# Kernel tuning notes

Measured on AMD Instinct MI355X. Metric: run time of the kernel, lower is better.

The kernel has to match this reference:

```python
import jax, jax.numpy as jnp
import numpy as np

B, N, DIM = 4, 2048, 1024
HEADS, DH = 16, 64
INNER = HEADS * DH
SCALE = 8.0
EPS = 1e-5


def setup_inputs() -> dict:
    key = jax.random.key(0)
    ks = jax.random.split(key, 8)
    x = jax.random.normal(ks[0], (B, N, DIM), dtype=jnp.float32)
    context_mask = jax.random.bernoulli(ks[1], 0.9, (B, N))
    gamma = jnp.ones((DIM,), dtype=jnp.float32)
    null_kv = jax.random.normal(ks[2], (2, HEADS, 1, DH), dtype=jnp.float32)
    Wq = jax.random.normal(ks[3], (DIM, INNER), dtype=jnp.float32) * 0.02
    Wkv = jax.random.normal(ks[4], (DIM, 2 * INNER), dtype=jnp.float32) * 0.02
    # q_scale init: scale / dim_head**-0.5 = 8 * sqrt(64) = 64
    q_scale = jnp.full((DH,), SCALE * (DH ** 0.5), dtype=jnp.float32)
    k_scale = jnp.ones((DH,), dtype=jnp.float32)
    Wout = jax.random.normal(ks[5], (INNER, DIM), dtype=jnp.float32) * 0.02
    return {"x": x, "context_mask": context_mask, "gamma": gamma,
            "null_kv": null_kv, "Wq": Wq, "Wkv": Wkv,
            "q_scale": q_scale, "k_scale": k_scale, "Wout": Wout}


def _l2norm(t):
    return t / jnp.sqrt(jnp.sum(t * t, axis=-1, keepdims=True) + 1e-12)


def reference(x, context_mask, gamma, null_kv, Wq, Wkv, q_scale, k_scale, Wout):
    b, n, _ = x.shape
    # LayerNorm (beta buffer is zeros)
    mu = jnp.mean(x, axis=-1, keepdims=True)
    var = jnp.mean((x - mu) ** 2, axis=-1, keepdims=True)
    xn = (x - mu) / jnp.sqrt(var + EPS) * gamma
    # projections
    q = (xn @ Wq).reshape(b, n, HEADS, DH)
    kv = xn @ Wkv
    k = kv[..., :INNER].reshape(b, n, HEADS, DH)
    v = kv[..., INNER:].reshape(b, n, HEADS, DH)
    # null kv token: [h,1,d] -> [b,1,h,d]
    nk = jnp.broadcast_to(null_kv[0].transpose(1, 0, 2)[None], (b, 1, HEADS, DH))
    nv = jnp.broadcast_to(null_kv[1].transpose(1, 0, 2)[None], (b, 1, HEADS, DH))
    k = jnp.concatenate([nk, k], axis=1)  # [b, n+1, h, d]
    v = jnp.concatenate([nv, v], axis=1)
    # cosine-sim attention with learned per-dim scales
    q = _l2norm(q) * q_scale
    k = _l2norm(k) * k_scale
    # bias from mask (padded True for null token)
    mask = jnp.pad(context_mask, ((0, 0), (1, 0)), constant_values=True)
    bias = jnp.where(mask, 0.0, -10000.0)[:, None, None, :]  # [b,1,1,n+1]
    # memory_efficient_attention applies 1/sqrt(dh) internally
    scores = jnp.einsum('bqhd,bkhd->bhqk', q, k) * (DH ** -0.5) + bias
    attn = jax.nn.softmax(scores, axis=-1)
    out = jnp.einsum('bhqk,bkhd->bqhd', attn, v).reshape(b, n, INNER)
    return out @ Wout
```

## Files before the change

kernel.cpp:

```cpp
#include <hip/hip_runtime.h>
#include <hip/hip_bf16.h>
#include <stdint.h>


using f32x4  = __attribute__((ext_vector_type(4))) float;
using bf16x8 = __attribute__((ext_vector_type(8))) __bf16;
using f16x8  = __attribute__((ext_vector_type(8))) _Float16;
using uintv4 = __attribute__((ext_vector_type(4))) unsigned int;

__device__ __forceinline__ float b2f(unsigned short u) {
    return __uint_as_float(((unsigned)u) << 16);
}
__device__ __forceinline__ unsigned short f2b(float f) {
    unsigned u = __float_as_uint(f);
    u += 0x7fffu + ((u >> 16) & 1u);
    return (unsigned short)(u >> 16);
}
__device__ __forceinline__ f32x4 mfma16(bf16x8 a, bf16x8 b, f32x4 c) {
    return __builtin_amdgcn_mfma_f32_16x16x32_bf16(a, b, c, 0, 0, 0);
}
__device__ __forceinline__ f32x4 mfma16h(f16x8 a, f16x8 b, f32x4 c) {
    return __builtin_amdgcn_mfma_f32_16x16x32_f16(a, b, c, 0, 0, 0);
}
__device__ __forceinline__ unsigned pk16(float a, float b) {
    return __builtin_bit_cast(unsigned, __builtin_amdgcn_cvt_pkrtz(a, b));
}
__device__ __forceinline__ void gl_lds16(const unsigned short* g, __bf16* l) {
    __builtin_amdgcn_global_load_lds(
        (const __attribute__((address_space(1))) unsigned int*)g,
        (__attribute__((address_space(3))) unsigned int*)l, 16, 0, 0);
}

__global__ __launch_bounds__(256) void transpose_f2b(
    const float* __restrict__ in, unsigned short* __restrict__ out,
    int R, int C)
{
    __shared__ unsigned short t[32][33];
    int tx = threadIdx.x, ty = threadIdx.y;
    int c = blockIdx.x * 32 + tx;
#pragma unroll
    for (int i = 0; i < 4; ++i) {
        int r = blockIdx.y * 32 + ty + i * 8;
        t[ty + i * 8][tx] = f2b(in[(size_t)r * C + c]);
    }
    __syncthreads();
    int r2 = blockIdx.y * 32 + tx;
#pragma unroll
    for (int i = 0; i < 4; ++i) {
        int c2 = blockIdx.x * 32 + ty + i * 8;
        out[(size_t)c2 * R + r2] = t[tx][ty + i * 8];
    }
}

__global__ __launch_bounds__(256) void ln_kernel(
    const float* __restrict__ x, const float* __restrict__ gamma,
    unsigned short* __restrict__ xn)
{
    int row = blockIdx.x, tid = threadIdx.x;
    int wave = tid >> 6, lane = tid & 63;
    float4 raw = *(const float4*)(x + ((size_t)row << 10) + (tid << 2));
    float v[4] = { raw.x, raw.y, raw.z, raw.w };
    float s  = v[0] + v[1] + v[2] + v[3];
    float s2 = v[0]*v[0] + v[1]*v[1] + v[2]*v[2] + v[3]*v[3];
#pragma unroll
    for (int off = 1; off < 64; off <<= 1) {
        s  += __shfl_xor(s, off);
        s2 += __shfl_xor(s2, off);
    }
    __shared__ float ps[4], ps2[4], sh[2];
    if (lane == 0) { ps[wave] = s; ps2[wave] = s2; }
    __syncthreads();
    if (tid == 0) {
        float S  = ps[0] + ps[1] + ps[2] + ps[3];
        float S2 = ps2[0] + ps2[1] + ps2[2] + ps2[3];
        float mu  = S * (1.f / 1024.f);
        float var = S2 * (1.f / 1024.f) - mu * mu;
        sh[0] = mu; sh[1] = rsqrtf(var + 1e-5f);
    }
    __syncthreads();
    float mu = sh[0], rstd = sh[1];
    float4 g4 = *(const float4*)(gamma + (tid << 2));
    float g[4] = { g4.x, g4.y, g4.z, g4.w };
    unsigned short o[4];
#pragma unroll
    for (int i = 0; i < 4; ++i) o[i] = f2b((v[i] - mu) * rstd * g[i]);
    uint2 out;
    out.x = (unsigned)o[0] | ((unsigned)o[1] << 16);
    out.y = (unsigned)o[2] | ((unsigned)o[3] << 16);
    *(uint2*)(xn + ((size_t)row << 10) + (tid << 2)) = out;
}

template<int MODE>
__global__ __launch_bounds__(256, 2) void gemm_bt(
    const unsigned short* __restrict__ A, const unsigned short* __restrict__ Bt,
    void* __restrict__ Cout, const float* __restrict__ scale,
    int M, int N, int K)
{
    __shared__ __bf16 As[128 * 32];
    __shared__ __bf16 Bs[128 * 32];
    int tid = threadIdx.x, lane = tid & 63, wave = tid >> 6;
    int quad = lane >> 4, l15 = lane & 15;
    int m0 = blockIdx.y * 128, n0 = blockIdx.x * 128;
    int wm = (wave & 1) * 64, wn = (wave >> 1) * 64;
    f32x4 acc[4][4] = {};

    const int srow = wave * 32 + (lane >> 2);
    const int scol = (lane & 3) << 3;
    const unsigned short* gA = A  + (size_t)(m0 + srow) * K + scol;
    const unsigned short* gB = Bt + (size_t)(n0 + srow) * K + scol;
    __bf16* lA0 = &As[(wave * 32) * 32];
    __bf16* lA1 = &As[(wave * 32 + 16) * 32];
    __bf16* lB0 = &Bs[(wave * 32) * 32];
    __bf16* lB1 = &Bs[(wave * 32 + 16) * 32];
    const size_t rstep = (size_t)16 * K;

    for (int k0 = 0; k0 < K; k0 += 32) {
        gl_lds16(gA,         lA0);
        gl_lds16(gA + rstep, lA1);
        gl_lds16(gB,         lB0);
        gl_lds16(gB + rstep, lB1);
        gA += 32; gB += 32;
        __syncthreads();
        bf16x8 af[4], bfv[4];
#pragma unroll
        for (int i = 0; i < 4; ++i)
            af[i] = *(const bf16x8*)&As[(wm + i * 16 + l15) * 32 + quad * 8];
#pragma unroll
        for (int j = 0; j < 4; ++j)
            bfv[j] = *(const bf16x8*)&Bs[(wn + j * 16 + l15) * 32 + quad * 8];
#pragma unroll
        for (int i = 0; i < 4; ++i)
#pragma unroll
            for (int j = 0; j < 4; ++j)
                acc[i][j] = mfma16(af[i], bfv[j], acc[i][j]);
        __syncthreads();
    }

    if (MODE == 2) {
#pragma unroll
        for (int i = 0; i < 4; ++i)
#pragma unroll
            for (int j = 0; j < 4; ++j) {
                int row = m0 + wm + i * 16 + quad * 4;
                int col = n0 + wn + j * 16 + l15;
                size_t base = (size_t)row * N + col;
#pragma unroll
                for (int r = 0; r < 4; ++r)
                    ((float*)Cout)[base + (size_t)r * N] = acc[i][j][r];
            }
        return;
    }

    const bool isv = (MODE == 1) && ((n0 + wn) >= 1024);
    float sc[4];
    if (!isv) {
#pragma unroll
        for (int j = 0; j < 4; ++j) {
            float s = scale[j * 16 + l15];
            sc[j] = (MODE == 0) ? s * (0.125f * 1.44269504088896f) : s;
        }
    }
#pragma unroll
    for (int i = 0; i < 4; ++i)
#pragma unroll
        for (int r = 0; r < 4; ++r) {
            float mul = 1.f;
            if (!isv) {
                float ss = 0.f;
#pragma unroll
                for (int j = 0; j < 4; ++j) ss += acc[i][j][r] * acc[i][j][r];
                ss += __shfl_xor(ss, 1); ss += __shfl_xor(ss, 2);
                ss += __shfl_xor(ss, 4); ss += __shfl_xor(ss, 8);
                mul = rsqrtf(ss + 1e-12f);
            }
            size_t rowbase = (size_t)(m0 + wm + i * 16 + quad * 4 + r) * N
                           + n0 + wn + l15;
#pragma unroll
            for (int j = 0; j < 4; ++j) {
                float v = acc[i][j][r];
                unsigned short w = isv
                    ? __builtin_bit_cast(unsigned short, (_Float16)v)
                    : f2b(v * mul * sc[j]);
                ((unsigned short*)Cout)[rowbase + j * 16] = w;
            }
        }
}

__global__ __launch_bounds__(256) void nullkv_kernel(
    const float* __restrict__ null_kv, const float* __restrict__ k_scale,
    unsigned short* __restrict__ knull, unsigned short* __restrict__ vnull)
{
    int wave = threadIdx.x >> 6, lane = threadIdx.x & 63;
    int h = blockIdx.x * 4 + wave;
    int idx = (h << 6) + lane;
    float kvl = null_kv[idx];
    float ss = kvl * kvl;
#pragma unroll
    for (int off = 1; off < 64; off <<= 1) ss += __shfl_xor(ss, off);
    knull[idx] = f2b(kvl * rsqrtf(ss + 1e-12f) * k_scale[lane]);
    vnull[idx] = __builtin_bit_cast(unsigned short, (_Float16)null_kv[1024 + idx]);
}

__global__ __launch_bounds__(256, 3) void attn_kernel(
    const unsigned short* __restrict__ qn,
    const unsigned short* __restrict__ kv,
    const unsigned short* __restrict__ knull,
    const unsigned short* __restrict__ vnull,
    const int* __restrict__ mask,
    unsigned short* __restrict__ ao)
{
    __shared__ __bf16 Kt[2][64 * 64];
    __shared__ unsigned int Vt32[64 * 34];
    __shared__ __align__(16) float biasLds[64];

    const int tid = threadIdx.x, lane = tid & 63, wave = tid >> 6;
    const int quad = lane >> 4, l15 = lane & 15;
    const int bh = blockIdx.x;
    const int b = bh >> 4, h = bh & 15;
    const int mbase = blockIdx.y * 128 + wave * 32;
    const size_t rowoff = (size_t)b * 2048;

    bf16x8 qf[2][2];
#pragma unroll
    for (int rg = 0; rg < 2; ++rg)
#pragma unroll
        for (int ks = 0; ks < 2; ++ks)
            qf[rg][ks] = *(const bf16x8*)
                &qn[((rowoff + mbase + rg * 16 + l15) << 10) + (h << 6) + ks * 32 + quad * 8];

    const int t8  = lane >> 3;
    const int ksc = ((lane & 7) ^ t8) << 3;

    uint2 va[2], vb[2]; float vmsk;

    auto kIssue = [&](int nt, int buf) {
#pragma unroll
        for (int p = 0; p < 2; ++p) {
            int r = wave * 16 + p * 8 + t8;
            int T = ((r >> 5) << 5) | (((r >> 2) & 3) << 3)
                  | (((r >> 4) & 1) << 2) | (r & 3);
            int j = (nt << 6) + T;
            int jr = j - 1; if (jr > 2047) jr = 2047;
            const unsigned short* src = (j == 0)
                ? knull + (h << 6) + ksc
                : kv + ((rowoff + (size_t)jr) << 11) + (h << 6) + ksc;
            gl_lds16(src, &Kt[buf][(wave * 16 + p * 8) * 64]);
        }
    };
    auto vPrefetch = [&](int nt) {
#pragma unroll
        for (int it = 0; it < 2; ++it) {
            int u = it * 256 + tid;
            int tp = u >> 4, d0 = (u & 15) << 2;
            int j0 = (nt << 6) + tp * 2;
            int jr0 = j0 - 1; if (jr0 > 2047) jr0 = 2047;
            int jr1 = j0;     if (jr1 > 2047) jr1 = 2047;
            const unsigned short* s0 = (j0 == 0)
                ? vnull + (h << 6) + d0
                : kv + ((rowoff + (size_t)jr0) << 11) + 1024 + (h << 6) + d0;
            const unsigned short* s1 =
                  kv + ((rowoff + (size_t)jr1) << 11) + 1024 + (h << 6) + d0;
            va[it] = *(const uint2*)s0;
            vb[it] = *(const uint2*)s1;
        }
        int j = (nt << 6) + tid;
        float bv = -512.f;
        if (j == 0 || (j <= 2048 && mask[b * 2048 + j - 1] != 0)) bv = 0.f;
        vmsk = bv;
    };
    auto vCommit = [&]() {
#pragma unroll
        for (int it = 0; it < 2; ++it) {
            int u = it * 256 + tid;
            int tp = u >> 4, d0 = (u & 15) << 2;
            unsigned ax = va[it].x, ay = va[it].y;
            unsigned bx = vb[it].x, by = vb[it].y;
            Vt32[(d0 + 0) * 34 + tp] = (ax & 0xffffu) | (bx << 16);
            Vt32[(d0 + 1) * 34 + tp] = (ax >> 16)     | (bx & 0xffff0000u);
            Vt32[(d0 + 2) * 34 + tp] = (ay & 0xffffu) | (by << 16);
            Vt32[(d0 + 3) * 34 + tp] = (ay >> 16)     | (by & 0xffff0000u);
        }
        if (tid < 64) biasLds[tid] = vmsk;
    };

    f32x4 O[2][4] = {};
    float rs[2] = {0.f, 0.f};

    kIssue(0, 0);
    vPrefetch(0);

    for (int nt = 0; nt < 33; ++nt) {
        const int buf = nt & 1;
        __syncthreads();
        vCommit();
        __syncthreads();
        if (nt < 32) {
            kIssue(nt + 1, buf ^ 1);
            vPrefetch(nt + 1);
        }

#pragma unroll
        for (int g = 0; g < 2; ++g) {
            float4 b0 = *(const float4*)&biasLds[(g << 5) + (quad << 3)];
            float4 b1 = *(const float4*)&biasLds[(g << 5) + (quad << 3) + 4];
            f32x4 s[2][2];
#pragma unroll
            for (int rg = 0; rg < 2; ++rg) {
                s[rg][0] = f32x4{ b0.x, b0.y, b0.z, b0.w };
                s[rg][1] = f32x4{ b1.x, b1.y, b1.z, b1.w };
            }
#pragma unroll
            for (int t = 0; t < 2; ++t) {
                const __bf16* kb = &Kt[buf][((g * 2 + t) * 16 + l15) * 64];
                bf16x8 k0 = *(const bf16x8*)&kb[(quad ^ (l15 & 7)) << 3];
                bf16x8 k1 = *(const bf16x8*)&kb[((4 + quad) ^ (l15 & 7)) << 3];
#pragma unroll
                for (int rg = 0; rg < 2; ++rg) {
                    s[rg][t] = mfma16(k0, qf[rg][0], s[rg][t]);
                    s[rg][t] = mfma16(k1, qf[rg][1], s[rg][t]);
                }
            }
            f16x8 vf8[4];
#pragma unroll
            for (int dt = 0; dt < 4; ++dt) {
                int cu = (dt * 16 + l15) * 34 + (g << 4) + (quad << 2);
                uint2 lo = *(const uint2*)&Vt32[cu];
                uint2 hi = *(const uint2*)&Vt32[cu + 2];
                uintv4 rv = { lo.x, lo.y, hi.x, hi.y };
                vf8[dt] = __builtin_bit_cast(f16x8, rv);
            }
#pragma unroll
            for (int rg = 0; rg < 2; ++rg) {
                float e0 = __builtin_amdgcn_exp2f(s[rg][0][0]);
                float e1 = __builtin_amdgcn_exp2f(s[rg][0][1]);
                float e2 = __builtin_amdgcn_exp2f(s[rg][0][2]);
                float e3 = __builtin_amdgcn_exp2f(s[rg][0][3]);
                float e4 = __builtin_amdgcn_exp2f(s[rg][1][0]);
                float e5 = __builtin_amdgcn_exp2f(s[rg][1][1]);
                float e6 = __builtin_amdgcn_exp2f(s[rg][1][2]);
                float e7 = __builtin_amdgcn_exp2f(s[rg][1][3]);
                rs[rg] += ((e0 + e1) + (e2 + e3)) + ((e4 + e5) + (e6 + e7));
                uintv4 pu = { pk16(e0, e1), pk16(e2, e3),
                              pk16(e4, e5), pk16(e6, e7) };
                f16x8 p = __builtin_bit_cast(f16x8, pu);
#pragma unroll
                for (int dt = 0; dt < 4; ++dt)
                    O[rg][dt] = mfma16h(p, vf8[dt], O[rg][dt]);
            }
        }
    }

#pragma unroll
    for (int rg = 0; rg < 2; ++rg) {
        rs[rg] += __shfl_xor(rs[rg], 16);
        rs[rg] += __shfl_xor(rs[rg], 32);
    }
#pragma unroll
    for (int rg = 0; rg < 2; ++rg) {
        float inv[4];
#pragma unroll
        for (int r = 0; r < 4; ++r)
            inv[r] = 1.f / __shfl(rs[rg], quad * 4 + r);
#pragma unroll
        for (int dt = 0; dt < 4; ++dt) {
            size_t base = ((rowoff + mbase + rg * 16 + quad * 4) << 10)
                        + (h << 6) + dt * 16 + l15;
#pragma unroll
            for (int r = 0; r < 4; ++r)
                ao[base + ((size_t)r << 10)] = f2b(O[rg][dt][r] * inv[r]);
        }
    }
}

extern "C" void kernel_launch(void* const* d_in, const int* in_sizes, int n_in,
                              void* d_out, int out_size, void* d_ws, size_t ws_size,
                              hipStream_t stream)
{
    const float* x       = (const float*)d_in[0];
    const int*   mask    = (const int*)d_in[1];
    const float* gamma   = (const float*)d_in[2];
    const float* null_kv = (const float*)d_in[3];
    const float* Wq      = (const float*)d_in[4];
    const float* Wkv     = (const float*)d_in[5];
    const float* q_scale = (const float*)d_in[6];
    const float* k_scale = (const float*)d_in[7];
    const float* Wout    = (const float*)d_in[8];

    char* ws = (char*)d_ws;
    unsigned short* xn    = (unsigned short*)(ws);
    unsigned short* ao    = xn;
    unsigned short* q     = (unsigned short*)(ws + (16u << 20));
    unsigned short* kvb   = (unsigned short*)(ws + (32u << 20));
    unsigned short* WqT   = (unsigned short*)(ws + (64u << 20));
    unsigned short* WkvT  = (unsigned short*)(ws + (66u << 20));
    unsigned short* WoutT = (unsigned short*)(ws + (70u << 20));
    unsigned short* knull = (unsigned short*)(ws + (72u << 20));
    unsigned short* vnull = (unsigned short*)(ws + (72u << 20) + 4096);

    dim3 tb(32, 8);
    transpose_f2b<<<dim3(32, 32), tb, 0, stream>>>(Wq,   WqT,   1024, 1024);
    transpose_f2b<<<dim3(64, 32), tb, 0, stream>>>(Wkv,  WkvT,  1024, 2048);
    transpose_f2b<<<dim3(32, 32), tb, 0, stream>>>(Wout, WoutT, 1024, 1024);

    ln_kernel<<<8192, 256, 0, stream>>>(x, gamma, xn);

    gemm_bt<0><<<dim3(8, 64),  256, 0, stream>>>(xn, WqT,  q,   q_scale, 8192, 1024, 1024);
    gemm_bt<1><<<dim3(16, 64), 256, 0, stream>>>(xn, WkvT, kvb, k_scale, 8192, 2048, 1024);

    nullkv_kernel<<<4, 256, 0, stream>>>(null_kv, k_scale, knull, vnull);

    attn_kernel<<<dim3(64, 16), 256, 0, stream>>>(q, kvb, knull, vnull, mask, ao);

    gemm_bt<2><<<dim3(8, 64), 256, 0, stream>>>(ao, WoutT, d_out, nullptr,
                                                8192, 1024, 1024);
}
```

Measured before the change: 314.2 us.

## Write V pre-transposed from KV GEMM and stream it into LDS asynchronously

The KV projection epilogue now writes V directly in a per-(batch,head) transposed [d][token] fp16 layout, padded to 2056 columns, with the null token in column 0 and zero-filled tail columns. The attention kernel then fetches V tiles with direct global-to-LDS loads into a double-buffered, XOR-swizzled layout. This removes the register prefetch, pack and commit transpose step and one barrier per tile. The cost is strided, poorly coalesced 2-byte scatter stores in the GEMM epilogue, plus extra workspace.

```diff
diff --git a/kernel.cpp b/kernel.cpp
--- a/kernel.cpp
+++ b/kernel.cpp
@@ -25,7 +25,7 @@
 __device__ __forceinline__ unsigned pk16(float a, float b) {
     return __builtin_bit_cast(unsigned, __builtin_amdgcn_cvt_pkrtz(a, b));
 }
-__device__ __forceinline__ void gl_lds16(const unsigned short* g, __bf16* l) {
+__device__ __forceinline__ void gl_lds16(const void* g, void* l) {
     __builtin_amdgcn_global_load_lds(
         (const __attribute__((address_space(1))) unsigned int*)g,
         (__attribute__((address_space(3))) unsigned int*)l, 16, 0, 0);
@@ -94,7 +94,8 @@
 __global__ __launch_bounds__(256, 2) void gemm_bt(
     const unsigned short* __restrict__ A, const unsigned short* __restrict__ Bt,
     void* __restrict__ Cout, const float* __restrict__ scale,
-    int M, int N, int K)
+    unsigned short* __restrict__ Vout,
+    int M, int N, int K, int ldc)
 {
     __shared__ __bf16 As[128 * 32];
     __shared__ __bf16 Bs[128 * 32];
@@ -143,52 +144,64 @@
             for (int j = 0; j < 4; ++j) {
                 int row = m0 + wm + i * 16 + quad * 4;
                 int col = n0 + wn + j * 16 + l15;
-                size_t base = (size_t)row * N + col;
+                size_t base = (size_t)row * ldc + col;
 #pragma unroll
                 for (int r = 0; r < 4; ++r)
-                    ((float*)Cout)[base + (size_t)r * N] = acc[i][j][r];
+                    ((float*)Cout)[base + (size_t)r * ldc] = acc[i][j][r];
             }
         return;
     }
 
     const bool isv = (MODE == 1) && ((n0 + wn) >= 1024);
+    if (MODE == 1 && isv) {
+        int hv = (n0 + wn - 1024) >> 6;
+#pragma unroll
+        for (int i = 0; i < 4; ++i)
+#pragma unroll
+            for (int r = 0; r < 4; ++r) {
+                int tok = m0 + wm + i * 16 + quad * 4 + r;
+                int b = tok >> 11;
+                int col = (tok & 2047) + 1;
+                size_t rowb = (size_t)(((b << 4) + hv) << 6);
+#pragma unroll
+                for (int j = 0; j < 4; ++j) {
+                    float v = acc[i][j][r];
+                    Vout[(rowb + j * 16 + l15) * 2056 + col] =
+                        __builtin_bit_cast(unsigned short, (_Float16)v);
+                }
+            }
+        return;
+    }
+
     float sc[4];
-    if (!isv) {
-#pragma unroll
-        for (int j = 0; j < 4; ++j) {
-            float s = scale[j * 16 + l15];
-            sc[j] = (MODE == 0) ? s * (0.125f * 1.44269504088896f) : s;
-        }
+#pragma unroll
+    for (int j = 0; j < 4; ++j) {
+        float s = scale[j * 16 + l15];
+        sc[j] = (MODE == 0) ? s * (0.125f * 1.44269504088896f) : s;
     }
 #pragma unroll
     for (int i = 0; i < 4; ++i)
 #pragma unroll
         for (int r = 0; r < 4; ++r) {
-            float mul = 1.f;
-            if (!isv) {
-                float ss = 0.f;
-#pragma unroll
-                for (int j = 0; j < 4; ++j) ss += acc[i][j][r] * acc[i][j][r];
-                ss += __shfl_xor(ss, 1); ss += __shfl_xor(ss, 2);
-                ss += __shfl_xor(ss, 4); ss += __shfl_xor(ss, 8);
-                mul = rsqrtf(ss + 1e-12f);
-            }
-            size_t rowbase = (size_t)(m0 + wm + i * 16 + quad * 4 + r) * N
+            float ss = 0.f;
+#pragma unroll
+            for (int j = 0; j < 4; ++j) ss += acc[i][j][r] * acc[i][j][r];
+            ss += __shfl_xor(ss, 1); ss += __shfl_xor(ss, 2);
+            ss += __shfl_xor(ss, 4); ss += __shfl_xor(ss, 8);
+            float mul = rsqrtf(ss + 1e-12f);
+            size_t rowbase = (size_t)(m0 + wm + i * 16 + quad * 4 + r) * ldc
                            + n0 + wn + l15;
 #pragma unroll
             for (int j = 0; j < 4; ++j) {
                 float v = acc[i][j][r];
-                unsigned short w = isv
-                    ? __builtin_bit_cast(unsigned short, (_Float16)v)
-                    : f2b(v * mul * sc[j]);
-                ((unsigned short*)Cout)[rowbase + j * 16] = w;
+                ((unsigned short*)Cout)[rowbase + j * 16] = f2b(v * mul * sc[j]);
             }
         }
 }
 
 __global__ __launch_bounds__(256) void nullkv_kernel(
     const float* __restrict__ null_kv, const float* __restrict__ k_scale,
-    unsigned short* __restrict__ knull, unsigned short* __restrict__ vnull)
+    unsigned short* __restrict__ knull, unsigned short* __restrict__ Vt)
 {
     int wave = threadIdx.x >> 6, lane = threadIdx.x & 63;
     int h = blockIdx.x * 4 + wave;
@@ -198,20 +211,31 @@
 #pragma unroll
     for (int off = 1; off < 64; off <<= 1) ss += __shfl_xor(ss, off);
     knull[idx] = f2b(kvl * rsqrtf(ss + 1e-12f) * k_scale[lane]);
-    vnull[idx] = __builtin_bit_cast(unsigned short, (_Float16)null_kv[1024 + idx]);
+    unsigned short vn =
+        __builtin_bit_cast(unsigned short, (_Float16)null_kv[1024 + idx]);
+#pragma unroll
+    for (int b = 0; b < 4; ++b)
+        Vt[((size_t)(((b << 4) + h) << 6) + lane) * 2056] = vn;
+    int t = blockIdx.x * 256 + threadIdx.x;
+    uintv4 z = { 0u, 0u, 0u, 0u };
+#pragma unroll
+    for (int rr = 0; rr < 4; ++rr) {
+        size_t row = (size_t)t * 4 + rr;
+        *(uintv4*)(Vt + row * 2056 + 2048) = z;
+    }
 }
 
 __global__ __launch_bounds__(256, 3) void attn_kernel(
     const unsigned short* __restrict__ qn,
-    const unsigned short* __restrict__ kv,
+    const unsigned short* __restrict__ kvK,
     const unsigned short* __restrict__ knull,
-    const unsigned short* __restrict__ vnull,
+    const unsigned short* __restrict__ Vt,
     const int* __restrict__ mask,
     unsigned short* __restrict__ ao)
 {
-    __shared__ __bf16 Kt[2][64 * 64];
-    __shared__ unsigned int Vt32[64 * 34];
-    __shared__ __align__(16) float biasLds[64];
+    __shared__ __bf16    Kt[2][64 * 64];
+    __shared__ _Float16  Vl[2][64 * 64];
+    __shared__ __align__(16) float biasLds[2][64];
 
     const int tid = threadIdx.x, lane = tid & 63, wave = tid >> 6;
     const int quad = lane >> 4, l15 = lane & 15;
@@ -229,9 +253,9 @@
                 &qn[((rowoff + mbase + rg * 16 + l15) << 10) + (h << 6) + ks * 32 + quad * 8];
 
     const int t8  = lane >> 3;
-    const int ksc = ((lane & 7) ^ t8) << 3;
-
-    uint2 va[2], vb[2]; float vmsk;
+    const int w7  = lane & 7;
+    const int ksc = (w7 ^ t8) << 3;
+    const size_t vrow0 = ((size_t)bh << 6);
 
     auto kIssue = [&](int nt, int buf) {
 #pragma unroll
@@ -243,66 +267,48 @@
             int jr = j - 1; if (jr > 2047) jr = 2047;
             const unsigned short* src = (j == 0)
                 ? knull + (h << 6) + ksc
-                : kv + ((rowoff + (size_t)jr) << 11) + (h << 6) + ksc;
+                : kvK + ((rowoff + (size_t)jr) << 10) + (h << 6) + ksc;
             gl_lds16(src, &Kt[buf][(wave * 16 + p * 8) * 64]);
         }
     };
-    auto vPrefetch = [&](int nt) {
-#pragma unroll
-        for (int it = 0; it < 2; ++it) {
-            int u = it * 256 + tid;
-            int tp = u >> 4, d0 = (u & 15) << 2;
-            int j0 = (nt << 6) + tp * 2;
-            int jr0 = j0 - 1; if (jr0 > 2047) jr0 = 2047;
-            int jr1 = j0;     if (jr1 > 2047) jr1 = 2047;
-            const unsigned short* s0 = (j0 == 0)
-                ? vnull + (h << 6) + d0
-                : kv + ((rowoff + (size_t)jr0) << 11) + 1024 + (h << 6) + d0;
-            const unsigned short* s1 =
-                  kv + ((rowoff + (size_t)jr1) << 11) + 1024 + (h << 6) + d0;
-            va[it] = *(const uint2*)s0;
-            vb[it] = *(const uint2*)s1;
-        }
+    auto vIssue = [&](int nt, int buf) {
+#pragma unroll
+        for (int p = 0; p < 2; ++p) {
+            int d = wave * 16 + p * 8 + t8;
+            int gsrc = (nt << 3) + (w7 ^ t8);
+            if (gsrc > 256) gsrc = 256;
+            const unsigned short* src = Vt + (vrow0 + d) * 2056 + (gsrc << 3);
+            gl_lds16(src, &Vl[buf][(wave * 16 + p * 8) * 64]);
+        }
+    };
+    auto biasFor = [&](int nt) -> float {
         int j = (nt << 6) + tid;
         float bv = -512.f;
         if (j == 0 || (j <= 2048 && mask[b * 2048 + j - 1] != 0)) bv = 0.f;
-        vmsk = bv;
-    };
-    auto vCommit = [&]() {
-#pragma unroll
-        for (int it = 0; it < 2; ++it) {
-            int u = it * 256 + tid;
-            int tp = u >> 4, d0 = (u & 15) << 2;
-            unsigned ax = va[it].x, ay = va[it].y;
-            unsigned bx = vb[it].x, by = vb[it].y;
-            Vt32[(d0 + 0) * 34 + tp] = (ax & 0xffffu) | (bx << 16);
-            Vt32[(d0 + 1) * 34 + tp] = (ax >> 16)     | (bx & 0xffff0000u);
-            Vt32[(d0 + 2) * 34 + tp] = (ay & 0xffffu) | (by << 16);
-            Vt32[(d0 + 3) * 34 + tp] = (ay >> 16)     | (by & 0xffff0000u);
-        }
-        if (tid < 64) biasLds[tid] = vmsk;
+        return bv;
     };
 
     f32x4 O[2][4] = {};
     float rs[2] = {0.f, 0.f};
 
     kIssue(0, 0);
-    vPrefetch(0);
+    vIssue(0, 0);
+    float bcur = biasFor(0);
 
     for (int nt = 0; nt < 33; ++nt) {
         const int buf = nt & 1;
-        __syncthreads();
-        vCommit();
+        if (tid < 64) biasLds[buf][tid] = bcur;
         __syncthreads();
         if (nt < 32) {
             kIssue(nt + 1, buf ^ 1);
-            vPrefetch(nt + 1);
+            vIssue(nt + 1, buf ^ 1);
+            bcur = biasFor(nt + 1);
         }
 
 #pragma unroll
         for (int g = 0; g < 2; ++g) {
-            float4 b0 = *(const float4*)&biasLds[(g << 5) + (quad << 3)];
-            float4 b1 = *(const float4*)&biasLds[(g << 5) + (quad << 3) + 4];
+            float4 b0 = *(const float4*)&biasLds[buf][(g << 5) + (quad << 3)];
+            float4 b1 = *(const float4*)&biasLds[buf][(g << 5) + (quad << 3) + 4];
             f32x4 s[2][2];
 #pragma unroll
             for (int rg = 0; rg < 2; ++rg) {
@@ -322,13 +328,10 @@
             }
             f16x8 vf8[4];
 #pragma unroll
-            for (int dt = 0; dt < 4; ++dt) {
-                int cu = (dt * 16 + l15) * 34 + (g << 4) + (quad << 2);
-                uint2 lo = *(const uint2*)&Vt32[cu];
-                uint2 hi = *(const uint2*)&Vt32[cu + 2];
-                uintv4 rv = { lo.x, lo.y, hi.x, hi.y };
-                vf8[dt] = __builtin_bit_cast(f16x8, rv);
-            }
+            for (int dt = 0; dt < 4; ++dt)
+                vf8[dt] = *(const f16x8*)
+                    &Vl[buf][(dt * 16 + l15) * 64
+                             + ((((g << 2) + quad) ^ (l15 & 7)) << 3)];
 #pragma unroll
             for (int rg = 0; rg < 2; ++rg) {
                 float e0 = __builtin_amdgcn_exp2f(s[rg][0][0]);
@@ -387,15 +390,17 @@
     const float* Wout    = (const float*)d_in[8];
 
     char* ws = (char*)d_ws;
+    const size_t VTG_OFF  = (size_t)48u << 20;
+    const size_t VTG_SIZE = (size_t)4096 * 4112;
     unsigned short* xn    = (unsigned short*)(ws);
     unsigned short* ao    = xn;
-    unsigned short* q     = (unsigned short*)(ws + (16u << 20));
-    unsigned short* kvb   = (unsigned short*)(ws + (32u << 20));
-    unsigned short* WqT   = (unsigned short*)(ws + (64u << 20));
-    unsigned short* WkvT  = (unsigned short*)(ws + (66u << 20));
-    unsigned short* WoutT = (unsigned short*)(ws + (70u << 20));
-    unsigned short* knull = (unsigned short*)(ws + (72u << 20));
-    unsigned short* vnull = (unsigned short*)(ws + (72u << 20) + 4096);
+    unsigned short* q     = (unsigned short*)(ws + ((size_t)16u << 20));
+    unsigned short* kvK   = (unsigned short*)(ws + ((size_t)32u << 20));
+    unsigned short* VtG   = (unsigned short*)(ws + VTG_OFF);
+    unsigned short* WqT   = (unsigned short*)(ws + VTG_OFF + VTG_SIZE - ((size_t)2u << 20));
+    unsigned short* WkvT  = (unsigned short*)(ws + VTG_OFF + VTG_SIZE);
+    unsigned short* WoutT = (unsigned short*)(ws + VTG_OFF + VTG_SIZE + ((size_t)4u << 20));
+    unsigned short* knull = (unsigned short*)(ws + VTG_OFF + VTG_SIZE + ((size_t)6u << 20));
 
     dim3 tb(32, 8);
     transpose_f2b<<<dim3(32, 32), tb, 0, stream>>>(Wq,   WqT,   1024, 1024);
@@ -404,13 +409,15 @@
 
     ln_kernel<<<8192, 256, 0, stream>>>(x, gamma, xn);
 
-    gemm_bt<0><<<dim3(8, 64),  256, 0, stream>>>(xn, WqT,  q,   q_scale, 8192, 1024, 1024);
-    gemm_bt<1><<<dim3(16, 64), 256, 0, stream>>>(xn, WkvT, kvb, k_scale, 8192, 2048, 1024);
-
-    nullkv_kernel<<<4, 256, 0, stream>>>(null_kv, k_scale, knull, vnull);
-
-    attn_kernel<<<dim3(64, 16), 256, 0, stream>>>(q, kvb, knull, vnull, mask, ao);
-
-    gemm_bt<2><<<dim3(8, 64), 256, 0, stream>>>(ao, WoutT, d_out, nullptr,
-                                                8192, 1024, 1024);
-}
+    gemm_bt<0><<<dim3(8, 64),  256, 0, stream>>>(xn, WqT, q, q_scale, nullptr,
+                                                 8192, 1024, 1024, 1024);
+    nullkv_kernel<<<4, 256, 0, stream>>>(null_kv, k_scale, knull, VtG);
+
+    gemm_bt<1><<<dim3(16, 64), 256, 0, stream>>>(xn, WkvT, kvK, k_scale, VtG,
+                                                 8192, 2048, 1024, 1024);
+
+    attn_kernel<<<dim3(64, 16), 256, 0, stream>>>(q, kvK, knull, VtG, mask, ao);
+
+    gemm_bt<2><<<dim3(8, 64), 256, 0, stream>>>(ao, WoutT, d_out, nullptr, nullptr,
+                                                8192, 1024, 1024, 1024);
+}
```

Result: no change. 313.6 us (-0.2%).
